# Kernel optimization log

Measured on AMD Instinct MI355X. Metric: run time of the kernel, lower is better.

## Reference

```python
import jax, jax.numpy as jnp
import numpy as np

N_NODES = 50000
N_EDGES = 1600000
HIDDEN = 64
HEADS = 8
EPS = 1e-16  # matches PyG segment-softmax denominator epsilon


def setup_inputs() -> dict:
    key = jax.random.key(0)
    ks = jax.random.split(key, 8)
    node_features = jax.random.normal(ks[0], (N_NODES,), dtype=jnp.float32)
    edge_index = jax.random.randint(ks[1], (2, N_EDGES), 0, N_NODES, dtype=jnp.int64)
    cycle_mask = jax.random.uniform(ks[2], (N_EDGES,), dtype=jnp.float32)
    # feature_proj: Linear(1, HIDDEN)
    W_proj = jax.random.normal(ks[3], (HIDDEN, 1), dtype=jnp.float32) * 0.5
    b_proj = jax.random.normal(ks[4], (HIDDEN,), dtype=jnp.float32) * 0.1
    # attention_net: Linear(2*HIDDEN+1, HEADS)
    fan_in = 2 * HIDDEN + 1
    W_att = jax.random.normal(ks[5], (HEADS, fan_in), dtype=jnp.float32) / np.sqrt(fan_in)
    b_att = jax.random.normal(ks[6], (HEADS,), dtype=jnp.float32) * 0.1
    cycle_penalty = jnp.full((HEADS,), -1.0, dtype=jnp.float32)
    min_sum_scaler = jnp.array([0.8], dtype=jnp.float32)
    return {
        "node_features": node_features,
        "cycle_mask": cycle_mask,
        "W_proj": W_proj,
        "b_proj": b_proj,
        "W_att": W_att,
        "b_att": b_att,
        "cycle_penalty": cycle_penalty,
        "min_sum_scaler": min_sum_scaler,
        "edge_index": edge_index,
    }


def reference(node_features, cycle_mask, W_proj, b_proj, W_att, b_att,
              cycle_penalty, min_sum_scaler, edge_index):
    src = edge_index[0]
    dst = edge_index[1]
    n = node_features.shape[0]
    w = W_proj[:, 0]  # [H]
    # per-edge projected features: [E, H]
    x_src = node_features[src][:, None] * w[None, :] + b_proj
    x_dst = node_features[dst][:, None] * w[None, :] + b_proj
    att_input = jnp.concatenate([x_src, x_dst, cycle_mask[:, None]], axis=-1)  # [E, 2H+1]
    raw = att_input @ W_att.T + b_att  # [E, heads]
    raw = jnp.where(raw >= 0, raw, 0.2 * raw)  # leaky_relu(0.2)
    raw = raw + cycle_mask[:, None] * cycle_penalty
    # segment softmax over edges grouped by dst
    seg_max = jax.ops.segment_max(raw, dst, num_segments=n)  # [N, heads]
    e = jnp.exp(raw - seg_max[dst])
    seg_sum = jax.ops.segment_sum(e, dst, num_segments=n)
    attn = e / (seg_sum[dst] + EPS)  # [E, heads]
    mean_attn = attn.mean(axis=-1)  # [E]
    messages = node_features[src] * mean_attn * min_sum_scaler[0]
    out = jax.ops.segment_sum(messages, dst, num_segments=n)
    return out
```

## Files before the change

### kernel.cpp

```cpp
#include <hip/hip_runtime.h>

#define N_NODES 50000
#define N_EDGES 1600000
#define HEADS 8
#define HIDDEN 64
#define FAN_IN (2*HIDDEN + 1)
#define EPSF 1e-16f

#define BBITS 8
#define BSIZE 256
#define NB 196
#define NSB 512
#define EPB 3125
#define NTS 256
#define NTR 512
#define CAP 12032

#define CNT_OFF   0
#define COLB_OFF  524288
#define TOT_OFF   1048576
#define PAY_OFF   2097152
#define DL_OFF    (PAY_OFF + (size_t)N_EDGES * 8)
#define WS_NEEDED (DL_OFF + (size_t)N_EDGES)

__global__ __launch_bounds__(NTS) void k_hist(const int* __restrict__ ei,
                                              int* __restrict__ cnt) {
    __shared__ int hist[NB];
    const int t = threadIdx.x, blk = blockIdx.x;
    if (t < NB) hist[t] = 0;
    __syncthreads();
    const int e0 = blk * EPB;
    for (int i = t; i < EPB; i += NTS)
        atomicAdd(&hist[((unsigned)ei[N_EDGES + e0 + i]) >> BBITS], 1);
    __syncthreads();
    if (t < NB) cnt[t * NSB + blk] = hist[t];
}

__global__ __launch_bounds__(NSB) void k_colscan(const int* __restrict__ cnt,
                                                 int* __restrict__ colbase,
                                                 int* __restrict__ tot) {
    __shared__ int lds[NSB];
    const int t = threadIdx.x, b = blockIdx.x;
    const int v = cnt[b * NSB + t];
    lds[t] = v;
    __syncthreads();
    for (int d = 1; d < NSB; d <<= 1) {
        const int x = (t >= d) ? lds[t - d] : 0;
        __syncthreads();
        lds[t] += x;
        __syncthreads();
    }
    colbase[b * NSB + t] = lds[t] - v;
    if (t == NSB - 1) tot[b] = lds[t];
}

__global__ __launch_bounds__(NTS) void k_scatter(const int* __restrict__ ei,
                                                 const float* __restrict__ cmask,
                                                 const float* __restrict__ nf,
                                                 const int* __restrict__ colbase,
                                                 const int* __restrict__ tot,
                                                 float2* __restrict__ pay,
                                                 unsigned char* __restrict__ dl8) {
    __shared__ int pr[EPB];
    __shared__ int inv[EPB];
    __shared__ int hist[NB];
    __shared__ int lstart[NB];
    __shared__ int cur[NB];
    __shared__ int scr[256];
    const int t = threadIdx.x, blk = blockIdx.x;
    const int e0 = blk * EPB;

    if (t < NB) hist[t] = 0;
    __syncthreads();

    for (int i = t; i < EPB; i += NTS) {
        const int dv = ei[N_EDGES + e0 + i];
        const int bkt = ((unsigned)dv) >> BBITS;
        const int rank = atomicAdd(&hist[bkt], 1);
        pr[i] = (bkt << 20) | ((dv & (BSIZE - 1)) << 12) | rank;
    }
    __syncthreads();

    int mytot = (t < NB) ? tot[t] : 0;
    scr[t] = mytot;
    __syncthreads();
    for (int d = 1; d < 256; d <<= 1) {
        const int x = (t >= d) ? scr[t - d] : 0;
        __syncthreads();
        scr[t] += x;
        __syncthreads();
    }
    const int bstart_t = scr[t] - mytot;
    __syncthreads();
    int myh = (t < NB) ? hist[t] : 0;
    scr[t] = myh;
    __syncthreads();
    for (int d = 1; d < 256; d <<= 1) {
        const int x = (t >= d) ? scr[t - d] : 0;
        __syncthreads();
        scr[t] += x;
        __syncthreads();
    }
    if (t < NB) {
        const int ls = scr[t] - myh;
        lstart[t] = ls;
        cur[t] = bstart_t + colbase[t * NSB + blk] - ls;
    }
    __syncthreads();

    for (int i = t; i < EPB; i += NTS) {
        const int u = pr[i];
        inv[lstart[u >> 20] + (u & 0xFFF)] = i;
    }
    __syncthreads();

    for (int p = t; p < EPB; p += NTS) {
        const int i = inv[p];
        const int u = pr[i];
        const int bkt = u >> 20;
        const int g = cur[bkt] + p;
        const int e = e0 + i;
        pay[g] = make_float2(nf[ei[e]], cmask[e]);
        dl8[g] = (unsigned char)((u >> 12) & 255);
    }
}

__global__ __launch_bounds__(NTR) void k_reduce(const float* __restrict__ nf,
                                                const float* __restrict__ Wp,
                                                const float* __restrict__ bp,
                                                const float* __restrict__ Wa,
                                                const float* __restrict__ ba,
                                                const float* __restrict__ cp,
                                                const float* __restrict__ sc,
                                                const int* __restrict__ tot,
                                                const float2* __restrict__ pay,
                                                const unsigned char* __restrict__ dl8,
                                                float* __restrict__ out) {
    __shared__ float2 pbuf[CAP];
    __shared__ int    hist[BSIZE];
    __shared__ int    noff[BSIZE + 1];
    __shared__ float  FD[BSIZE];
    __shared__ float  cstl[40];
    __shared__ int    scr[256];
    __shared__ int    sI0;
    const int t = threadIdx.x, b = blockIdx.x;

    {
        const int k = t >> 6, j = t & 63;
        const float* row = Wa + k * FAN_IN;
        const float w = Wp[j], bb = bp[j];
        const float r1 = row[j], r2 = row[HIDDEN + j];
        float a1 = w * r1, a2 = w * r2, d = bb * (r1 + r2);
        #pragma unroll
        for (int s = 32; s > 0; s >>= 1) {
            a1 += __shfl_xor(a1, s);
            a2 += __shfl_xor(a2, s);
            d  += __shfl_xor(d, s);
        }
        if (j == 0) {
            cstl[k]      = a1;
            cstl[8 + k]  = a2;
            cstl[16 + k] = row[2 * HIDDEN];
            cstl[24 + k] = d + ba[k];
            cstl[32 + k] = cp[k];
        }
    }

    {
        int v = 0;
        if (t < 256) v = (t < NB) ? tot[t] : 0;
        if (t < 256) scr[t] = v;
        __syncthreads();
        for (int d = 1; d < 256; d <<= 1) {
            int x = 0;
            if (t < 256 && t >= d) x = scr[t - d];
            __syncthreads();
            if (t < 256 && t >= d) scr[t] += x;
            __syncthreads();
        }
        if (t == b) sI0 = scr[t] - v;
        __syncthreads();
    }
    const int i0 = sI0;
    const int i1 = i0 + tot[b];

    if (t < BSIZE) {
        hist[t] = 0;
        const int n = b * BSIZE + t;
        FD[t] = (n < N_NODES) ? nf[n] : 0.f;
    }
    if (t == 0) noff[0] = 0;
    __syncthreads();

    for (int i = i0 + t; i < i1; i += NTR)
        atomicAdd(&hist[dl8[i]], 1);
    __syncthreads();
    if (t < BSIZE) noff[t + 1] = hist[t];
    __syncthreads();
    for (int d = 1; d < BSIZE; d <<= 1) {
        int v = 0;
        if (t < BSIZE && t >= d) v = noff[t + 1 - d];
        __syncthreads();
        if (t < BSIZE && t >= d) noff[t + 1] += v;
        __syncthreads();
    }
    if (t < BSIZE) hist[t] = noff[t];
    __syncthreads();

    for (int i = i0 + t; i < i1; i += NTR) {
        const int dl = dl8[i];
        const int p = atomicAdd(&hist[dl], 1);
        if (p < CAP) pbuf[p] = pay[i];
    }
    __syncthreads();

    float A1[8], A2[8], CC[8], DD[8], PP[8];
    #pragma unroll
    for (int k = 0; k < 8; ++k) {
        A1[k] = cstl[k];      A2[k] = cstl[8 + k];  CC[k] = cstl[16 + k];
        DD[k] = cstl[24 + k]; PP[k] = cstl[32 + k];
    }
    const int j = t >> 1, par = t & 1;
    const int n = b * BSIZE + j;
    if (n < N_NODES) {
        const int lo = min(noff[j], CAP), hi = min(noff[j + 1], CAP);
        const float fd = FD[j];
        float as[8], at[8];
        #pragma unroll
        for (int k = 0; k < 8; ++k) { as[k] = 0.f; at[k] = 0.f; }
        for (int i = lo + par; i < hi; i += 2) {
            const float2 p = pbuf[i];
            #pragma unroll
            for (int k = 0; k < 8; ++k) {
                float r = p.x * A1[k] + fd * A2[k] + p.y * CC[k] + DD[k];
                r = (r >= 0.f) ? r : 0.2f * r;
                r += p.y * PP[k];
                const float ev = __expf(r);
                as[k] += ev;
                at[k] += p.x * ev;
            }
        }
        #pragma unroll
        for (int k = 0; k < 8; ++k) {
            as[k] += __shfl_xor(as[k], 1);
            at[k] += __shfl_xor(at[k], 1);
        }
        if (par == 0) {
            float acc = 0.f;
            #pragma unroll
            for (int k = 0; k < 8; ++k) acc += at[k] / (as[k] + EPSF);
            out[n] = acc * 0.125f * sc[0];
        }
    }
}

__global__ __launch_bounds__(256) void cagat_edge_atomic(
    const float* __restrict__ nf, const float* __restrict__ cmask,
    const float* __restrict__ Wp, const float* __restrict__ bp,
    const float* __restrict__ Wa, const float* __restrict__ ba,
    const float* __restrict__ cp, const int* __restrict__ ei,
    float* __restrict__ S, float* __restrict__ T) {
    __shared__ float A1[HEADS], A2[HEADS], CC[HEADS], DD[HEADS], PP[HEADS];
    const int t = threadIdx.x;
    if (t < HEADS) {
        const float* row = Wa + t * FAN_IN;
        float a1 = 0.f, a2 = 0.f, d = 0.f;
        for (int h = 0; h < HIDDEN; ++h) {
            float w = Wp[h], b = bp[h];
            a1 += w * row[h]; a2 += w * row[HIDDEN + h];
            d += b * (row[h] + row[HIDDEN + h]);
        }
        A1[t] = a1; A2[t] = a2; CC[t] = row[2*HIDDEN]; DD[t] = d + ba[t]; PP[t] = cp[t];
    }
    __syncthreads();
    const int e = blockIdx.x * 256 + t;
    if (e >= N_EDGES) return;
    const int src = ei[e], dst = ei[N_EDGES + e];
    const float fs = nf[src], fd = nf[dst], c = cmask[e];
    #pragma unroll
    for (int k = 0; k < HEADS; ++k) {
        float r = fs * A1[k] + fd * A2[k] + c * CC[k] + DD[k];
        r = (r >= 0.f) ? r : 0.2f * r;
        r += c * PP[k];
        float ev = __expf(r);
        atomicAdd(S + dst * HEADS + k, ev);
        atomicAdd(T + dst * HEADS + k, fs * ev);
    }
}

__global__ __launch_bounds__(256) void cagat_node_atomic(
    const float* __restrict__ S, const float* __restrict__ T,
    const float* __restrict__ scaler, float* __restrict__ out) {
    const int n = blockIdx.x * 256 + threadIdx.x;
    if (n >= N_NODES) return;
    float acc = 0.f;
    #pragma unroll
    for (int k = 0; k < HEADS; ++k)
        acc += T[n * HEADS + k] / (S[n * HEADS + k] + EPSF);
    out[n] = acc * 0.125f * scaler[0];
}

extern "C" void kernel_launch(void* const* d_in, const int* in_sizes, int n_in,
                              void* d_out, int out_size, void* d_ws, size_t ws_size,
                              hipStream_t stream) {
    const float* nf    = (const float*)d_in[0];
    const float* cmask = (const float*)d_in[1];
    const float* Wp    = (const float*)d_in[2];
    const float* bp    = (const float*)d_in[3];
    const float* Wa    = (const float*)d_in[4];
    const float* ba    = (const float*)d_in[5];
    const float* cp    = (const float*)d_in[6];
    const float* sc    = (const float*)d_in[7];
    const int*   ei    = (const int*)d_in[8];

    char* ws = (char*)d_ws;

    if (ws_size >= WS_NEEDED) {
        int*           cnt     = (int*)(ws + CNT_OFF);
        int*           colbase = (int*)(ws + COLB_OFF);
        int*           tot     = (int*)(ws + TOT_OFF);
        float2*        pay     = (float2*)(ws + PAY_OFF);
        unsigned char* dl      = (unsigned char*)(ws + DL_OFF);

        k_hist<<<NSB, NTS, 0, stream>>>(ei, cnt);
        k_colscan<<<NB, NSB, 0, stream>>>(cnt, colbase, tot);
        k_scatter<<<NSB, NTS, 0, stream>>>(ei, cmask, nf, colbase, tot, pay, dl);
        k_reduce<<<NB, NTR, 0, stream>>>(nf, Wp, bp, Wa, ba, cp, sc, tot, pay, dl,
                                         (float*)d_out);
    } else {
        float* S = (float*)d_ws;
        float* T = S + (size_t)N_NODES * HEADS;
        hipMemsetAsync(d_ws, 0, (size_t)N_NODES * HEADS * 2 * sizeof(float), stream);
        cagat_edge_atomic<<<(N_EDGES + 255) / 256, 256, 0, stream>>>(
            nf, cmask, Wp, bp, Wa, ba, cp, ei, S, T);
        cagat_node_atomic<<<(N_NODES + 255) / 256, 256, 0, stream>>>(
            S, T, sc, (float*)d_out);
    }
}
```

Measured before the change: 131.7 us.

## Shrink destination buckets to 64 nodes and precompute bucket starts

Destination buckets shrink from 256 to 64 nodes, so there are 782 buckets and 782 reduce blocks of 256 threads, each with a much smaller LDS payload buffer. The scatter kernel scans 1024 entries and writes the global bucket start offsets once, so each reduce block no longer rescans the totals. The reduce kernel caches the local destination bytes in LDS between its two passes and gives each node four threads instead of two. The goal is more parallelism and occupancy in the reduce stage, at the cost of larger histogram and column-scan work in the earlier kernels and a lower per-bucket capacity cap.

```diff
diff --git a/kernel.cpp b/kernel.cpp
--- a/kernel.cpp
+++ b/kernel.cpp
@@ -7,33 +7,53 @@
 #define FAN_IN (2*HIDDEN + 1)
 #define EPSF 1e-16f
 
-#define BBITS 8
-#define BSIZE 256
-#define NB 196
+#define BBITS 6
+#define BSIZE 64
+#define NB 782
+#define NBPAD 1024
 #define NSB 512
 #define EPB 3125
 #define NTS 256
-#define NTR 512
-#define CAP 12032
+#define NTR 256
+#define CAP 3072
 
 #define CNT_OFF   0
-#define COLB_OFF  524288
-#define TOT_OFF   1048576
-#define PAY_OFF   2097152
+#define COLB_OFF  2097152
+#define TOT_OFF   4194304
+#define BST_OFF   4202496
+#define PAY_OFF   8388608
 #define DL_OFF    (PAY_OFF + (size_t)N_EDGES * 8)
 #define WS_NEEDED (DL_OFF + (size_t)N_EDGES)
+
+__device__ inline void scan1024(int* scn, int* scr, int t) {
+    int v[4]; int s = 0;
+    #pragma unroll
+    for (int q = 0; q < 4; ++q) { v[q] = scn[t * 4 + q]; s += v[q]; }
+    scr[t] = s;
+    __syncthreads();
+    for (int d = 1; d < 256; d <<= 1) {
+        const int x = (t >= d) ? scr[t - d] : 0;
+        __syncthreads();
+        scr[t] += x;
+        __syncthreads();
+    }
+    int run = scr[t] - s;
+    #pragma unroll
+    for (int q = 0; q < 4; ++q) { scn[t * 4 + q] = run; run += v[q]; }
+    __syncthreads();
+}
 
 __global__ __launch_bounds__(NTS) void k_hist(const int* __restrict__ ei,
                                               int* __restrict__ cnt) {
     __shared__ int hist[NB];
     const int t = threadIdx.x, blk = blockIdx.x;
-    if (t < NB) hist[t] = 0;
+    for (int i = t; i < NB; i += NTS) hist[i] = 0;
     __syncthreads();
     const int e0 = blk * EPB;
     for (int i = t; i < EPB; i += NTS)
         atomicAdd(&hist[((unsigned)ei[N_EDGES + e0 + i]) >> BBITS], 1);
     __syncthreads();
-    if (t < NB) cnt[t * NSB + blk] = hist[t];
+    for (int i = t; i < NB; i += NTS) cnt[i * NSB + blk] = hist[i];
 }
 
 __global__ __launch_bounds__(NSB) void k_colscan(const int* __restrict__ cnt,
@@ -59,69 +79,69 @@
                                                  const float* __restrict__ nf,
                                                  const int* __restrict__ colbase,
                                                  const int* __restrict__ tot,
+                                                 int* __restrict__ bstart,
                                                  float2* __restrict__ pay,
                                                  unsigned char* __restrict__ dl8) {
-    __shared__ int pr[EPB];
-    __shared__ int inv[EPB];
-    __shared__ int hist[NB];
-    __shared__ int lstart[NB];
-    __shared__ int cur[NB];
-    __shared__ int scr[256];
+    __shared__ int            pr[EPB];
+    __shared__ unsigned short inv[EPB];
+    __shared__ int            histL[NB];
+    __shared__ int            curG[NB];
+    __shared__ int            scn[NBPAD];
+    __shared__ int            scr[256];
     const int t = threadIdx.x, blk = blockIdx.x;
     const int e0 = blk * EPB;
 
-    if (t < NB) hist[t] = 0;
+    for (int i = t; i < NB; i += NTS) histL[i] = 0;
     __syncthreads();
 
     for (int i = t; i < EPB; i += NTS) {
         const int dv = ei[N_EDGES + e0 + i];
         const int bkt = ((unsigned)dv) >> BBITS;
-        const int rank = atomicAdd(&hist[bkt], 1);
-        pr[i] = (bkt << 20) | ((dv & (BSIZE - 1)) << 12) | rank;
-    }
-    __syncthreads();
-
-    int mytot = (t < NB) ? tot[t] : 0;
-    scr[t] = mytot;
-    __syncthreads();
-    for (int d = 1; d < 256; d <<= 1) {
-        const int x = (t >= d) ? scr[t - d] : 0;
-        __syncthreads();
-        scr[t] += x;
-        __syncthreads();
-    }
-    const int bstart_t = scr[t] - mytot;
-    __syncthreads();
-    int myh = (t < NB) ? hist[t] : 0;
-    scr[t] = myh;
-    __syncthreads();
-    for (int d = 1; d < 256; d <<= 1) {
-        const int x = (t >= d) ? scr[t - d] : 0;
-        __syncthreads();
-        scr[t] += x;
-        __syncthreads();
-    }
-    if (t < NB) {
-        const int ls = scr[t] - myh;
-        lstart[t] = ls;
-        cur[t] = bstart_t + colbase[t * NSB + blk] - ls;
-    }
+        const int rank = atomicAdd(&histL[bkt], 1);
+        pr[i] = (bkt << 18) | ((dv & (BSIZE - 1)) << 12) | rank;
+    }
+    __syncthreads();
+
+    #pragma unroll
+    for (int q = 0; q < 4; ++q) {
+        const int x = t * 4 + q;
+        scn[x] = (x < NB) ? tot[x] : 0;
+    }
+    __syncthreads();
+    scan1024(scn, scr, t);
+    if (blk == 0) {
+        #pragma unroll
+        for (int q = 0; q < 4; ++q) {
+            const int x = t * 4 + q;
+            if (x < NB) bstart[x] = scn[x];
+        }
+    }
+    for (int x = t; x < NB; x += NTS) curG[x] = scn[x] + colbase[x * NSB + blk];
+    __syncthreads();
+
+    #pragma unroll
+    for (int q = 0; q < 4; ++q) {
+        const int x = t * 4 + q;
+        scn[x] = (x < NB) ? histL[x] : 0;
+    }
+    __syncthreads();
+    scan1024(scn, scr, t);
+    for (int x = t; x < NB; x += NTS) curG[x] -= scn[x];
     __syncthreads();
 
     for (int i = t; i < EPB; i += NTS) {
         const int u = pr[i];
-        inv[lstart[u >> 20] + (u & 0xFFF)] = i;
+        inv[scn[u >> 18] + (u & 0xFFF)] = (unsigned short)i;
     }
     __syncthreads();
 
     for (int p = t; p < EPB; p += NTS) {
         const int i = inv[p];
         const int u = pr[i];
-        const int bkt = u >> 20;
-        const int g = cur[bkt] + p;
+        const int g = curG[u >> 18] + p;
         const int e = e0 + i;
         pay[g] = make_float2(nf[ei[e]], cmask[e]);
-        dl8[g] = (unsigned char)((u >> 12) & 255);
+        dl8[g] = (unsigned char)((u >> 12) & (BSIZE - 1));
     }
 }
 
@@ -133,26 +153,29 @@
                                                 const float* __restrict__ cp,
                                                 const float* __restrict__ sc,
                                                 const int* __restrict__ tot,
+                                                const int* __restrict__ bstart,
                                                 const float2* __restrict__ pay,
                                                 const unsigned char* __restrict__ dl8,
                                                 float* __restrict__ out) {
-    __shared__ float2 pbuf[CAP];
-    __shared__ int    hist[BSIZE];
-    __shared__ int    noff[BSIZE + 1];
-    __shared__ float  FD[BSIZE];
-    __shared__ float  cstl[40];
-    __shared__ int    scr[256];
-    __shared__ int    sI0;
+    __shared__ float2        pbuf[CAP];
+    __shared__ unsigned char dl_l[CAP];
+    __shared__ int           histN[BSIZE];
+    __shared__ int           noff[BSIZE + 1];
+    __shared__ float         FD[BSIZE];
+    __shared__ float         cstl[40];
     const int t = threadIdx.x, b = blockIdx.x;
 
     {
-        const int k = t >> 6, j = t & 63;
+        const int k = t >> 5, j = t & 31;
         const float* row = Wa + k * FAN_IN;
-        const float w = Wp[j], bb = bp[j];
+        const float w1 = Wp[j], b1 = bp[j], w2 = Wp[j + 32], b2 = bp[j + 32];
         const float r1 = row[j], r2 = row[HIDDEN + j];
-        float a1 = w * r1, a2 = w * r2, d = bb * (r1 + r2);
+        const float r3 = row[j + 32], r4 = row[HIDDEN + j + 32];
+        float a1 = w1 * r1 + w2 * r3;
+        float a2 = w1 * r2 + w2 * r4;
+        float d  = b1 * (r1 + r2) + b2 * (r3 + r4);
         #pragma unroll
-        for (int s = 32; s > 0; s >>= 1) {
+        for (int s = 16; s > 0; s >>= 1) {
             a1 += __shfl_xor(a1, s);
             a2 += __shfl_xor(a2, s);
             d  += __shfl_xor(d, s);
@@ -166,36 +189,24 @@
         }
     }
 
-    {
-        int v = 0;
-        if (t < 256) v = (t < NB) ? tot[t] : 0;
-        if (t < 256) scr[t] = v;
-        __syncthreads();
-        for (int d = 1; d < 256; d <<= 1) {
-            int x = 0;
-            if (t < 256 && t >= d) x = scr[t - d];
-            __syncthreads();
-            if (t < 256 && t >= d) scr[t] += x;
-            __syncthreads();
-        }
-        if (t == b) sI0 = scr[t] - v;
-        __syncthreads();
-    }
-    const int i0 = sI0;
-    const int i1 = i0 + tot[b];
+    const int i0 = bstart[b];
+    const int lenc = min(tot[b], CAP);
 
     if (t < BSIZE) {
-        hist[t] = 0;
+        histN[t] = 0;
         const int n = b * BSIZE + t;
         FD[t] = (n < N_NODES) ? nf[n] : 0.f;
     }
     if (t == 0) noff[0] = 0;
     __syncthreads();
 
-    for (int i = i0 + t; i < i1; i += NTR)
-        atomicAdd(&hist[dl8[i]], 1);
-    __syncthreads();
-    if (t < BSIZE) noff[t + 1] = hist[t];
+    for (int idx = t; idx < lenc; idx += NTR) {
+        const int d8 = dl8[i0 + idx];
+        dl_l[idx] = (unsigned char)d8;
+        atomicAdd(&histN[d8], 1);
+    }
+    __syncthreads();
+    if (t < BSIZE) noff[t + 1] = histN[t];
     __syncthreads();
     for (int d = 1; d < BSIZE; d <<= 1) {
         int v = 0;
@@ -204,13 +215,13 @@
         if (t < BSIZE && t >= d) noff[t + 1] += v;
         __syncthreads();
     }
-    if (t < BSIZE) hist[t] = noff[t];
-    __syncthreads();
-
-    for (int i = i0 + t; i < i1; i += NTR) {
-        const int dl = dl8[i];
-        const int p = atomicAdd(&hist[dl], 1);
-        if (p < CAP) pbuf[p] = pay[i];
+    if (t < BSIZE) histN[t] = noff[t];
+    __syncthreads();
+
+    for (int idx = t; idx < lenc; idx += NTR) {
+        const int d8 = dl_l[idx];
+        const int p = atomicAdd(&histN[d8], 1);
+        pbuf[p] = pay[i0 + idx];
     }
     __syncthreads();
 
@@ -220,37 +231,37 @@
         A1[k] = cstl[k];      A2[k] = cstl[8 + k];  CC[k] = cstl[16 + k];
         DD[k] = cstl[24 + k]; PP[k] = cstl[32 + k];
     }
-    const int j = t >> 1, par = t & 1;
+    const int j = t >> 2, par = t & 3;
     const int n = b * BSIZE + j;
-    if (n < N_NODES) {
-        const int lo = min(noff[j], CAP), hi = min(noff[j + 1], CAP);
-        const float fd = FD[j];
-        float as[8], at[8];
-        #pragma unroll
-        for (int k = 0; k < 8; ++k) { as[k] = 0.f; at[k] = 0.f; }
-        for (int i = lo + par; i < hi; i += 2) {
-            const float2 p = pbuf[i];
-            #pragma unroll
-            for (int k = 0; k < 8; ++k) {
-                float r = p.x * A1[k] + fd * A2[k] + p.y * CC[k] + DD[k];
-                r = (r >= 0.f) ? r : 0.2f * r;
-                r += p.y * PP[k];
-                const float ev = __expf(r);
-                as[k] += ev;
-                at[k] += p.x * ev;
-            }
-        }
+    const int lo = noff[j], hi = noff[j + 1];
+    const float fd = FD[j];
+    float as[8], at[8];
+    #pragma unroll
+    for (int k = 0; k < 8; ++k) { as[k] = 0.f; at[k] = 0.f; }
+    for (int i = lo + par; i < hi; i += 4) {
+        const float2 p = pbuf[i];
         #pragma unroll
         for (int k = 0; k < 8; ++k) {
-            as[k] += __shfl_xor(as[k], 1);
-            at[k] += __shfl_xor(at[k], 1);
-        }
-        if (par == 0) {
-            float acc = 0.f;
-            #pragma unroll
-            for (int k = 0; k < 8; ++k) acc += at[k] / (as[k] + EPSF);
-            out[n] = acc * 0.125f * sc[0];
-        }
+            float r = p.x * A1[k] + fd * A2[k] + p.y * CC[k] + DD[k];
+            r = (r >= 0.f) ? r : 0.2f * r;
+            r += p.y * PP[k];
+            const float ev = __expf(r);
+            as[k] += ev;
+            at[k] += p.x * ev;
+        }
+    }
+    #pragma unroll
+    for (int k = 0; k < 8; ++k) {
+        as[k] += __shfl_xor(as[k], 1);
+        at[k] += __shfl_xor(at[k], 1);
+        as[k] += __shfl_xor(as[k], 2);
+        at[k] += __shfl_xor(at[k], 2);
+    }
+    if (par == 0 && n < N_NODES) {
+        float acc = 0.f;
+        #pragma unroll
+        for (int k = 0; k < 8; ++k) acc += at[k] / (as[k] + EPSF);
+        out[n] = acc * 0.125f * sc[0];
     }
 }
 
@@ -319,14 +330,15 @@
         int*           cnt     = (int*)(ws + CNT_OFF);
         int*           colbase = (int*)(ws + COLB_OFF);
         int*           tot     = (int*)(ws + TOT_OFF);
+        int*           bstart  = (int*)(ws + BST_OFF);
         float2*        pay     = (float2*)(ws + PAY_OFF);
         unsigned char* dl      = (unsigned char*)(ws + DL_OFF);
 
         k_hist<<<NSB, NTS, 0, stream>>>(ei, cnt);
         k_colscan<<<NB, NSB, 0, stream>>>(cnt, colbase, tot);
-        k_scatter<<<NSB, NTS, 0, stream>>>(ei, cmask, nf, colbase, tot, pay, dl);
-        k_reduce<<<NB, NTR, 0, stream>>>(nf, Wp, bp, Wa, ba, cp, sc, tot, pay, dl,
-                                         (float*)d_out);
+        k_scatter<<<NSB, NTS, 0, stream>>>(ei, cmask, nf, colbase, tot, bstart, pay, dl);
+        k_reduce<<<NB, NTR, 0, stream>>>(nf, Wp, bp, Wa, ba, cp, sc, tot, bstart,
+                                         pay, dl, (float*)d_out);
     } else {
         float* S = (float*)d_ws;
         float* T = S + (size_t)N_NODES * HEADS;
```

Result: slower. 134.9 us (+2.4%).
